# Kernel optimization log

Measured on AMD Instinct MI355X. Metric: run time of the kernel, lower is better.

Reference implementation:

```python
import jax, jax.numpy as jnp
import numpy as np

NUM_HEADS = 4
NUM_EXPERTS = 8
TOP_K = 2
AUX_W = 0.1


def setup_inputs() -> dict:
    key = jax.random.key(0)
    ks = jax.random.split(key, 16)
    B, W, C, T = 32, 64, 27, 2000
    E_EEG, H, S = 200, 256, 768
    D2 = 2 * H  # MoE input/hidden dim = 512
    s = 0.02

    def p(k, shape):
        return (jax.random.normal(k, shape, jnp.float32) * s)

    z = lambda *shape: jnp.zeros(shape, jnp.float32)
    return {
        "eeg_windows": jax.random.normal(ks[0], (B, W, C, T), jnp.float32),
        "padding_mask": jnp.zeros((B, W), bool),
        "smiles_emb": jax.random.normal(ks[1], (B, S), jnp.float32),
        # window encoder (linear stand-in): flatten (C*T) -> E_EEG
        "enc_W": p(ks[2], (C * T, E_EEG)), "enc_b": z(E_EEG),
        # aggregator (masked-mean + linear stand-in): E_EEG -> H
        "agg_W": p(ks[3], (E_EEG, H)), "agg_b": z(H),
        # smiles projection
        "smiles_W": p(ks[4], (S, H)), "smiles_b": z(H),
        # cross attention
        "Wq": p(ks[5], (H, H)), "bq": z(H),
        "Wk": p(ks[6], (H, H)), "bk": z(H),
        "Wv": p(ks[7], (H, H)), "bv": z(H),
        "Wo": p(ks[8], (H, H)), "bo": z(H),
        # MoE gate + experts
        "gate_W": p(ks[9], (D2, NUM_EXPERTS)), "gate_b": z(NUM_EXPERTS),
        "exp_W1": p(ks[10], (NUM_EXPERTS, D2, D2)), "exp_b1": z(NUM_EXPERTS, D2),
        "exp_W2": p(ks[11], (NUM_EXPERTS, D2, H)), "exp_b2": z(NUM_EXPERTS, H),
        # classifier
        "ln_g": jnp.ones((H,), jnp.float32), "ln_b": z(H),
        "cls_W": p(ks[12], (H, 2)), "cls_b": z(2),
    }


def reference(eeg_windows, padding_mask, smiles_emb, enc_W, enc_b, agg_W, agg_b,
              smiles_W, smiles_b, Wq, bq, Wk, bk, Wv, bv, Wo, bo,
              gate_W, gate_b, exp_W1, exp_b1, exp_W2, exp_b2,
              ln_g, ln_b, cls_W, cls_b):
    B, W, C, T = eeg_windows.shape
    H = agg_W.shape[1]
    dh = H // NUM_HEADS

    # --- window encoding (stand-in linear encoder) ---
    wemb = eeg_windows.reshape(B, W, C * T) @ enc_W + enc_b  # (B, W, E_EEG)

    # --- aggregator: masked mean pool over windows, then project ---
    valid = (~padding_mask).astype(wemb.dtype)[..., None]      # (B, W, 1)
    pooled = (wemb * valid).sum(1) / jnp.maximum(valid.sum(1), 1.0)
    eeg_emb = pooled @ agg_W + agg_b                           # (B, H)

    smiles_proj = smiles_emb @ smiles_W + smiles_b             # (B, H)

    # --- cross attention (single query token over single kv token) ---
    q = (eeg_emb @ Wq + bq).reshape(B, NUM_HEADS, dh)
    k = (smiles_proj @ Wk + bk).reshape(B, NUM_HEADS, dh)
    v = (smiles_proj @ Wv + bv).reshape(B, NUM_HEADS, dh)
    scores = (q * k).sum(-1, keepdims=True) / jnp.sqrt(jnp.float32(dh))
    attn = jnp.exp(scores - scores)  # softmax over a single key == 1
    attended = (attn * v).reshape(B, H) @ Wo + bo              # (B, H)

    fused = jnp.concatenate([attended, smiles_proj], axis=-1)  # (B, 2H)

    # --- sparse MoE: dense experts, top-k gate, gather, combine ---
    gate_probs = jax.nn.softmax(fused @ gate_W + gate_b, axis=-1)  # (B, E)
    topk_p, topk_i = jax.lax.top_k(gate_probs, TOP_K)
    topk_p = topk_p / topk_p.sum(-1, keepdims=True)
    h1 = jax.nn.gelu(jnp.einsum('bd,edh->beh', fused, exp_W1) + exp_b1,
                     approximate=False)
    expert_out = jnp.einsum('beh,eho->beo', h1, exp_W2) + exp_b2   # (B, E, H)
    sel = jnp.take_along_axis(expert_out, topk_i[:, :, None], axis=1)
    moe_out = (sel * topk_p[..., None]).sum(1)                     # (B, H)

    usage = gate_probs.mean(0)
    uniform = jnp.ones_like(usage) / usage.shape[-1]
    aux = (usage * jnp.log(uniform) - jnp.log(usage) * uniform).sum()

    # --- classifier: LayerNorm + Linear ---
    mu = moe_out.mean(-1, keepdims=True)
    var = moe_out.var(-1, keepdims=True)
    xn = (moe_out - mu) / jnp.sqrt(var + 1e-5)
    logits = (xn * ln_g + ln_b) @ cls_W + cls_b                    # (B, 2)
    return logits, aux * AUX_W
```

## Files before the change

kernel.cpp:

```cpp
#include <hip/hip_runtime.h>
#include <math.h>

#define HD 256
#define SD 768
#define D2 512
#define NE 8
#define NB 32
#define NBLK 256
#define NTHR 256
#define SFP 516

typedef float f32x4 __attribute__((ext_vector_type(4)));
typedef unsigned u32x4 __attribute__((ext_vector_type(4)));

__device__ __forceinline__ float gelu_exact(float x) {
    return 0.5f * x * (1.0f + erff(x * 0.70710678118654752f));
}

__device__ __forceinline__ void cstf(float* p, float v) {
    __hip_atomic_store(p, v, __ATOMIC_RELAXED, __HIP_MEMORY_SCOPE_AGENT);
}
__device__ __forceinline__ float cldf(const float* p) {
    return __hip_atomic_load(p, __ATOMIC_RELAXED, __HIP_MEMORY_SCOPE_AGENT);
}
__device__ __forceinline__ void csti(int* p, int v) {
    __hip_atomic_store(p, v, __ATOMIC_RELAXED, __HIP_MEMORY_SCOPE_AGENT);
}
__device__ __forceinline__ int cldi(const int* p) {
    return __hip_atomic_load(p, __ATOMIC_RELAXED, __HIP_MEMORY_SCOPE_AGENT);
}

__device__ __forceinline__ void stage16k(const float* __restrict__ gsrc,
                                         float* __restrict__ lds, int t)
{
    const f32x4* src = (const f32x4*)gsrc;
    f32x4 r[16];
    #pragma unroll
    for (int j = 0; j < 16; ++j) {
        const f32x4* p = src + (t + j * 256);
        asm volatile("global_load_dwordx4 %0, %1, off sc0 sc1"
                     : "=v"(r[j]) : "v"(p));
    }
    asm volatile("s_waitcnt vmcnt(0)" ::: "memory");
    __builtin_amdgcn_sched_barrier(0);
    #pragma unroll
    for (int j = 0; j < 16; ++j) {
        int q = t + j * 256;
        *(f32x4*)&lds[(q >> 7) * SFP + (q & 127) * 4] = r[j];
    }
}

__device__ __forceinline__ void post_slot(unsigned* slots, unsigned tok) {
    __syncthreads();
    if (threadIdx.x == 0)
        __hip_atomic_store(slots + blockIdx.x, tok, __ATOMIC_RELAXED,
                           __HIP_MEMORY_SCOPE_AGENT);
}

__device__ __forceinline__ void finish_full(const unsigned* slots,
                                            unsigned* gen, unsigned tok) {
    const int t = threadIdx.x;
    if (blockIdx.x == 0) {
        if (t < 64) {
            const u32x4* p = (const u32x4*)slots + t;
            for (;;) {
                u32x4 v;
                asm volatile("global_load_dwordx4 %0, %1, off sc0 sc1\n\t"
                             "s_waitcnt vmcnt(0)"
                             : "=&v"(v) : "v"(p) : "memory");
                bool ok = (v[0] == tok) & (v[1] == tok) &
                          (v[2] == tok) & (v[3] == tok);
                if (__ballot(ok) == ~0ull) break;
                __builtin_amdgcn_s_sleep(1);
            }
            if (t == 0)
                __hip_atomic_store(gen, tok, __ATOMIC_RELAXED,
                                   __HIP_MEMORY_SCOPE_AGENT);
        }
    } else {
        if (t == 0) {
            while (__hip_atomic_load(gen, __ATOMIC_RELAXED,
                                     __HIP_MEMORY_SCOPE_AGENT) != tok)
                __builtin_amdgcn_s_sleep(1);
        }
    }
    __builtin_amdgcn_fence(__ATOMIC_ACQUIRE, "workgroup");
    __syncthreads();
}

__device__ __forceinline__ void wait_subset(const unsigned* slots, int nq,
                                            unsigned tok) {
    if ((int)threadIdx.x < nq) {
        const u32x4* p = (const u32x4*)slots + threadIdx.x;
        for (;;) {
            u32x4 v;
            asm volatile("global_load_dwordx4 %0, %1, off sc0 sc1\n\t"
                         "s_waitcnt vmcnt(0)"
                         : "=&v"(v) : "v"(p) : "memory");
            if ((v[0] == tok) & (v[1] == tok) & (v[2] == tok) & (v[3] == tok))
                break;
            __builtin_amdgcn_s_sleep(2);
        }
    }
    __builtin_amdgcn_fence(__ATOMIC_ACQUIRE, "workgroup");
    __syncthreads();
}

#define S_F     0
#define S_W     16512
#define S_R2    (16512 + 8192)
#define S_RED   (16512 + 8192 + 4096)
#define S_SMALL (16512 + 8192 + 4096 + 256)
#define SMEM_F  (16512 + 8192 + 4096 + 256 + 16)

__global__ __launch_bounds__(256) void fused_all(
    const float* __restrict__ smiles,
    const float* __restrict__ sW, const float* __restrict__ sb,
    const float* __restrict__ Wv, const float* __restrict__ bv,
    const float* __restrict__ Wo, const float* __restrict__ bo,
    const float* __restrict__ gW, const float* __restrict__ gb,
    const float* __restrict__ W1, const float* __restrict__ b1,
    const float* __restrict__ W2, const float* __restrict__ b2,
    const float* __restrict__ lng, const float* __restrict__ lnb,
    const float* __restrict__ clsW, const float* __restrict__ clsb,
    float* __restrict__ proj, float* __restrict__ fused,
    float* __restrict__ probs, float* __restrict__ pn,
    int* __restrict__ sel, float* __restrict__ h1,
    float* __restrict__ eo,
    unsigned* __restrict__ slot0, unsigned* __restrict__ slot1,
    unsigned* __restrict__ slot2, unsigned* __restrict__ slot3,
    unsigned* __restrict__ gen, unsigned* __restrict__ LC,
    float* __restrict__ out)
{
    __shared__ __align__(16) float smem[SMEM_F];
    __shared__ unsigned s_lc;
    const int bid = blockIdx.x, t = threadIdx.x;

    if (t == 0)
        s_lc = __hip_atomic_load(LC, __ATOMIC_RELAXED, __HIP_MEMORY_SCOPE_AGENT);
    __syncthreads();
    const unsigned tb = s_lc * 2654435761u;

    {
        int r = bid >> 3, sl = bid & 7;
        float* s_in = smem + S_F;
        float* s_red = smem + S_RED;
        const float* srow = smiles + (size_t)r * SD;
        for (int i = t; i < SD / 4; i += NTHR)
            ((float4*)s_in)[i] = ((const float4*)srow)[i];
        __syncthreads();
        int c = t & 31, kq = t >> 5;
        float acc = 0.f;
        const float* wp = sW + (size_t)(kq * 96) * HD + sl * 32 + c;
        #pragma unroll 8
        for (int k = 0; k < 96; ++k)
            acc = fmaf(s_in[kq * 96 + k], wp[(size_t)k * HD], acc);
        s_red[t] = acc;
        __syncthreads();
        if (t < 32) {
            float s = 0.f;
            #pragma unroll
            for (int q = 0; q < 8; ++q) s += s_red[q * 32 + t];
            int col = sl * 32 + t;
            s += sb[col];
            cstf(proj + r * HD + col, s);
            cstf(fused + (size_t)r * 2 * HD + HD + col, s);
        }
    }
    post_slot(slot0, tb + 1u);

    if (bid < NB) {
        wait_subset(slot0 + bid * 8, 2, tb + 1u);
        int b = bid;
        float* s_p   = smem + S_F;
        float* s_v   = smem + S_F + 256;
        float* s_f2  = smem + S_F + 512;
        float* s_acc = smem + S_R2;
        float* s_red = smem + S_RED;
        float* s_gate = smem + S_SMALL;
        s_p[t] = cldf(proj + b * HD + t);
        __syncthreads();
        int ks = t >> 6, cg = t & 63;

        f32x4 av = {0.f, 0.f, 0.f, 0.f};
        #pragma unroll 16
        for (int kk = 0; kk < 64; ++kk) {
            int k = ks * 64 + kk;
            f32x4 w = *(const f32x4*)(Wv + (size_t)k * HD + cg * 4);
            av += s_p[k] * w;
        }
        *(f32x4*)&s_acc[ks * 256 + cg * 4] = av;
        __syncthreads();
        s_v[t] = s_acc[t] + s_acc[256 + t] + s_acc[512 + t] + s_acc[768 + t]
               + bv[t];
        __syncthreads();

        f32x4 ao = {0.f, 0.f, 0.f, 0.f};
        #pragma unroll 16
        for (int kk = 0; kk < 64; ++kk) {
            int k = ks * 64 + kk;
            f32x4 w = *(const f32x4*)(Wo + (size_t)k * HD + cg * 4);
            ao += s_v[k] * w;
        }
        *(f32x4*)&s_acc[ks * 256 + cg * 4] = ao;
        __syncthreads();
        float att = s_acc[t] + s_acc[256 + t] + s_acc[512 + t] + s_acc[768 + t]
                  + bo[t];
        s_f2[t] = att;
        s_f2[HD + t] = s_p[t];
        cstf(fused + (size_t)b * 2 * HD + t, att);
        __syncthreads();

        int e = t & 7, ch = t >> 3;
        float gp = 0.f;
        #pragma unroll
        for (int j = 0; j < 16; ++j) {
            int d = ch * 16 + j;
            gp = fmaf(s_f2[d], gW[d * NE + e], gp);
        }
        s_red[t] = gp;
        __syncthreads();
        for (int off = 128; off >= 8; off >>= 1) {
            if (t < off) s_red[t] += s_red[t + off];
            __syncthreads();
        }
        if (t < NE) s_gate[t] = s_red[t] + gb[t];
        __syncthreads();
        if (t == 0) {
            float m = s_gate[0];
            for (int i = 1; i < NE; ++i) m = fmaxf(m, s_gate[i]);
            float ex[NE], ssum = 0.f;
            for (int i = 0; i < NE; ++i) { ex[i] = expf(s_gate[i] - m); ssum += ex[i]; }
            float pr[NE];
            for (int i = 0; i < NE; ++i) { pr[i] = ex[i] / ssum; cstf(probs + b * NE + i, pr[i]); }
            int i1 = 0;
            for (int i = 1; i < NE; ++i) if (pr[i] > pr[i1]) i1 = i;
            int i2 = (i1 == 0) ? 1 : 0;
            for (int i = 0; i < NE; ++i) if (i != i1 && pr[i] > pr[i2]) i2 = i;
            float p1 = pr[i1], p2 = pr[i2], s12 = p1 + p2;
            csti(sel + b * 2 + 0, i1);
            csti(sel + b * 2 + 1, i2);
            cstf(pn + b * 2 + 0, p1 / s12);
            cstf(pn + b * 2 + 1, p2 / s12);
        }
    }
    post_slot(slot1, tb + 2u);

    {
        int e = bid >> 5, ct = bid & 31;
        float* s_w = smem + S_W;
        const float* Wb = W1 + (size_t)e * D2 * D2 + ct * 16;
        #pragma unroll
        for (int j = 0; j < 8; ++j) {
            int q = t + j * 256;
            int k = q >> 2, c4 = (q & 3) * 4;
            *(float4*)&s_w[k * 16 + c4] = *(const float4*)(Wb + (size_t)k * D2 + c4);
        }
    }
    finish_full(slot1, gen + 0, tb + 2u);

    {
        int e = bid >> 5, ct = bid & 31;
        float* s_f  = smem + S_F;
        float* s_w  = smem + S_W;
        float* s_r2 = smem + S_R2;
        stage16k(fused, s_f, t);
        __syncthreads();
        int ks = t >> 5, l = t & 31;
        int rg = l >> 2, c4g = l & 3;
        const float* wb = s_w + c4g * 4;
        int k0 = ks * 64;
        f32x4 a0 = {0.f,0.f,0.f,0.f}, a1 = a0, a2 = a0, a3 = a0;
        #pragma unroll 2
        for (int kq = 0; kq < 16; ++kq) {
            int k = k0 + kq * 4;
            f32x4 w0 = *(const f32x4*)&wb[(k + 0) * 16];
            f32x4 w1 = *(const f32x4*)&wb[(k + 1) * 16];
            f32x4 w2 = *(const f32x4*)&wb[(k + 2) * 16];
            f32x4 w3 = *(const f32x4*)&wb[(k + 3) * 16];
            f32x4 f0 = *(const f32x4*)&s_f[(rg     ) * SFP + k];
            f32x4 f1 = *(const f32x4*)&s_f[(rg +  8) * SFP + k];
            f32x4 f2 = *(const f32x4*)&s_f[(rg + 16) * SFP + k];
            f32x4 f3 = *(const f32x4*)&s_f[(rg + 24) * SFP + k];
            a0 += f0[0]*w0 + f0[1]*w1 + f0[2]*w2 + f0[3]*w3;
            a1 += f1[0]*w0 + f1[1]*w1 + f1[2]*w2 + f1[3]*w3;
            a2 += f2[0]*w0 + f2[1]*w1 + f2[2]*w2 + f2[3]*w3;
            a3 += f3[0]*w0 + f3[1]*w1 + f3[2]*w2 + f3[3]*w3;
        }
        *(f32x4*)&s_r2[ks * 512 + (rg     ) * 16 + c4g * 4] = a0;
        *(f32x4*)&s_r2[ks * 512 + (rg +  8) * 16 + c4g * 4] = a1;
        *(f32x4*)&s_r2[ks * 512 + (rg + 16) * 16 + c4g * 4] = a2;
        *(f32x4*)&s_r2[ks * 512 + (rg + 24) * 16 + c4g * 4] = a3;
        __syncthreads();
        #pragma unroll
        for (int o = 0; o < 2; ++o) {
            int outi = t * 2 + o;
            float s = 0.f;
            #pragma unroll
            for (int p = 0; p < 8; ++p) s += s_r2[p * 512 + outi];
            int r = outi >> 4, cl = outi & 15;
            int col = ct * 16 + cl;
            cstf(h1 + ((size_t)e * NB + r) * D2 + col,
                 gelu_exact(s + b1[e * D2 + col]));
        }
    }
    post_slot(slot2, tb + 3u);

    if (bid >= 128) {
        post_slot(slot3, tb + 4u);
        return;
    }

    {
        int e = bid >> 4, ct = bid & 15;
        float* s_w = smem + S_W;
        const float* Wb = W2 + (size_t)e * D2 * HD + ct * 16;
        #pragma unroll
        for (int j = 0; j < 8; ++j) {
            int q = t + j * 256;
            int k = q >> 2, c4 = (q & 3) * 4;
            *(float4*)&s_w[k * 16 + c4] = *(const float4*)(Wb + (size_t)k * HD + c4);
        }
    }
    finish_full(slot2, gen + 1, tb + 3u);

    {
        int e = bid >> 4, ct = bid & 15;
        float* s_f  = smem + S_F;
        float* s_w  = smem + S_W;
        float* s_r2 = smem + S_R2;
        stage16k(h1 + (size_t)e * NB * D2, s_f, t);
        __syncthreads();
        int ks = t >> 5, l = t & 31;
        int rg = l >> 2, c4g = l & 3;
        const float* wb = s_w + c4g * 4;
        int k0 = ks * 64;
        f32x4 a0 = {0.f,0.f,0.f,0.f}, a1 = a0, a2 = a0, a3 = a0;
        #pragma unroll 2
        for (int kq = 0; kq < 16; ++kq) {
            int k = k0 + kq * 4;
            f32x4 w0 = *(const f32x4*)&wb[(k + 0) * 16];
            f32x4 w1 = *(const f32x4*)&wb[(k + 1) * 16];
            f32x4 w2 = *(const f32x4*)&wb[(k + 2) * 16];
            f32x4 w3 = *(const f32x4*)&wb[(k + 3) * 16];
            f32x4 f0 = *(const f32x4*)&s_f[(rg     ) * SFP + k];
            f32x4 f1 = *(const f32x4*)&s_f[(rg +  8) * SFP + k];
            f32x4 f2 = *(const f32x4*)&s_f[(rg + 16) * SFP + k];
            f32x4 f3 = *(const f32x4*)&s_f[(rg + 24) * SFP + k];
            a0 += f0[0]*w0 + f0[1]*w1 + f0[2]*w2 + f0[3]*w3;
            a1 += f1[0]*w0 + f1[1]*w1 + f1[2]*w2 + f1[3]*w3;
            a2 += f2[0]*w0 + f2[1]*w1 + f2[2]*w2 + f2[3]*w3;
            a3 += f3[0]*w0 + f3[1]*w1 + f3[2]*w2 + f3[3]*w3;
        }
        *(f32x4*)&s_r2[ks * 512 + (rg     ) * 16 + c4g * 4] = a0;
        *(f32x4*)&s_r2[ks * 512 + (rg +  8) * 16 + c4g * 4] = a1;
        *(f32x4*)&s_r2[ks * 512 + (rg + 16) * 16 + c4g * 4] = a2;
        *(f32x4*)&s_r2[ks * 512 + (rg + 24) * 16 + c4g * 4] = a3;
        __syncthreads();
        #pragma unroll
        for (int o = 0; o < 2; ++o) {
            int outi = t * 2 + o;
            float s = 0.f;
            #pragma unroll
            for (int p = 0; p < 8; ++p) s += s_r2[p * 512 + outi];
            int r = outi >> 4, cl = outi & 15;
            int col = ct * 16 + cl;
            cstf(eo + ((size_t)e * NB + r) * HD + col, s + b2[e * HD + col]);
        }
    }
    post_slot(slot3, tb + 4u);
    if (bid >= NB) return;

    finish_full(slot3, gen + 2, tb + 4u);

    {
        int b = bid;
        float* s_red = smem + S_RED;
        float* s_stats = smem + S_SMALL;
        int e0 = cldi(sel + b * 2 + 0), e1 = cldi(sel + b * 2 + 1);
        float p0 = cldf(pn + b * 2 + 0), p1 = cldf(pn + b * 2 + 1);
        float moe = p0 * cldf(eo + ((size_t)e0 * NB + b) * HD + t)
                  + p1 * cldf(eo + ((size_t)e1 * NB + b) * HD + t);

        s_red[t] = moe; __syncthreads();
        for (int off = 128; off > 0; off >>= 1) {
            if (t < off) s_red[t] += s_red[t + off];
            __syncthreads();
        }
        if (t == 0) s_stats[0] = s_red[0] * (1.f / HD);
        __syncthreads();
        float mu = s_stats[0];
        float d = moe - mu;

        s_red[t] = d * d; __syncthreads();
        for (int off = 128; off > 0; off >>= 1) {
            if (t < off) s_red[t] += s_red[t + off];
            __syncthreads();
        }
        if (t == 0) s_stats[1] = s_red[0] * (1.f / HD);
        __syncthreads();

        float xn = d * rsqrtf(s_stats[1] + 1e-5f);
        float y = fmaf(xn, lng[t], lnb[t]);

        s_red[t] = y * clsW[t * 2 + 0]; __syncthreads();
        for (int off = 128; off > 0; off >>= 1) {
            if (t < off) s_red[t] += s_red[t + off];
            __syncthreads();
        }
        if (t == 0) s_stats[2] = s_red[0] + clsb[0];
        __syncthreads();

        s_red[t] = y * clsW[t * 2 + 1]; __syncthreads();
        for (int off = 128; off > 0; off >>= 1) {
            if (t < off) s_red[t] += s_red[t + off];
            __syncthreads();
        }
        if (t == 0) {
            out[b * 2 + 0] = s_stats[2];
            out[b * 2 + 1] = s_red[0] + clsb[1];
        }

        if (bid == 0) {
            __syncthreads();
            s_red[t] = cldf(probs + t);
            __syncthreads();
            for (int off = 128; off >= 8; off >>= 1) {
                if (t < off) s_red[t] += s_red[t + off];
                __syncthreads();
            }
            if (t == 0) {
                float aux = 0.f;
                for (int e = 0; e < NE; ++e) {
                    float u = s_red[e] * (1.f / 32.f);
                    aux += u * logf(0.125f) - logf(u) * 0.125f;
                }
                out[64] = 0.1f * aux;
            }
        }
    }

    if (bid == 0 && t == 0)
        __hip_atomic_store(LC, s_lc + 1u, __ATOMIC_RELAXED,
                           __HIP_MEMORY_SCOPE_AGENT);
}

extern "C" void kernel_launch(void* const* d_in, const int* in_sizes, int n_in,
                              void* d_out, int out_size, void* d_ws, size_t ws_size,
                              hipStream_t stream) {
    (void)in_sizes; (void)n_in; (void)out_size; (void)ws_size;
    const float* smiles = (const float*)d_in[2];
    const float* sW  = (const float*)d_in[7];
    const float* sb  = (const float*)d_in[8];
    const float* Wv  = (const float*)d_in[13];
    const float* bv  = (const float*)d_in[14];
    const float* Wo  = (const float*)d_in[15];
    const float* bo  = (const float*)d_in[16];
    const float* gW  = (const float*)d_in[17];
    const float* gb  = (const float*)d_in[18];
    const float* W1  = (const float*)d_in[19];
    const float* b1  = (const float*)d_in[20];
    const float* W2  = (const float*)d_in[21];
    const float* b2  = (const float*)d_in[22];
    const float* lng = (const float*)d_in[23];
    const float* lnb = (const float*)d_in[24];
    const float* cW  = (const float*)d_in[25];
    const float* cb  = (const float*)d_in[26];
    float* out = (float*)d_out;
    float* ws  = (float*)d_ws;

    float*    proj  = ws;
    float*    fused = ws + 8192;
    float*    probs = ws + 24576;
    float*    pn    = ws + 24832;
    int*      sel   = (int*)(ws + 24896);
    float*    h1    = ws + 24960;
    float*    eo    = ws + 156032;
    unsigned* slot0 = (unsigned*)(ws + 221568);
    unsigned* slot1 = (unsigned*)(ws + 221824);
    unsigned* slot2 = (unsigned*)(ws + 222080);
    unsigned* slot3 = (unsigned*)(ws + 222336);
    unsigned* gen   = (unsigned*)(ws + 222592);
    unsigned* LC    = (unsigned*)(ws + 222596);

    fused_all<<<NBLK, NTHR, 0, stream>>>(
        smiles, sW, sb, Wv, bv, Wo, bo, gW, gb, W1, b1, W2, b2,
        lng, lnb, cW, cb,
        proj, fused, probs, pn, sel, h1, eo,
        slot0, slot1, slot2, slot3, gen, LC, out);
}
```

Before: 38.82 us.

## Replace full grid barriers with per-expert dependency waits in MoE stages

Swaps the grid-wide barriers before the second expert GEMM and the combine stage for targeted waits. Each expert-W2 block now waits only on the slot2 flags of the 16 blocks that produced its expert's h1. Each batch row waits only on the slot3 flags for its two selected experts. Block 0 also waits on all slot2 slots before bumping the launch counter, so slot reuse across launches stays safe. This removes stalls on unrelated blocks, but correctness now depends on the slot indexing matching the producer layout.

```diff
diff --git a/kernel.cpp b/kernel.cpp
--- a/kernel.cpp
+++ b/kernel.cpp
@@ -92,6 +92,25 @@
                                             unsigned tok) {
     if ((int)threadIdx.x < nq) {
         const u32x4* p = (const u32x4*)slots + threadIdx.x;
+        for (;;) {
+            u32x4 v;
+            asm volatile("global_load_dwordx4 %0, %1, off sc0 sc1\n\t"
+                         "s_waitcnt vmcnt(0)"
+                         : "=&v"(v) : "v"(p) : "memory");
+            if ((v[0] == tok) & (v[1] == tok) & (v[2] == tok) & (v[3] == tok))
+                break;
+            __builtin_amdgcn_s_sleep(2);
+        }
+    }
+    __builtin_amdgcn_fence(__ATOMIC_ACQUIRE, "workgroup");
+    __syncthreads();
+}
+
+__device__ __forceinline__ void wait_two_experts(const unsigned* slots,
+                                                 int ea, int eb, unsigned tok) {
+    if (threadIdx.x < 8) {
+        int es = (threadIdx.x < 4) ? ea : eb;
+        const u32x4* p = (const u32x4*)slots + es * 4 + (threadIdx.x & 3);
         for (;;) {
             u32x4 v;
             asm volatile("global_load_dwordx4 %0, %1, off sc0 sc1\n\t"
@@ -305,11 +324,7 @@
         }
     }
     post_slot(slot2, tb + 3u);
-
-    if (bid >= 128) {
-        post_slot(slot3, tb + 4u);
-        return;
-    }
+    if (bid >= 128) return;
 
     {
         int e = bid >> 4, ct = bid & 15;
@@ -322,7 +337,10 @@
             *(float4*)&s_w[k * 16 + c4] = *(const float4*)(Wb + (size_t)k * HD + c4);
         }
     }
-    finish_full(slot2, gen + 1, tb + 3u);
+    {
+        int e = bid >> 4;
+        wait_subset(slot2 + e * 32, 8, tb + 3u);
+    }
 
     {
         int e = bid >> 4, ct = bid & 15;
@@ -371,14 +389,15 @@
     post_slot(slot3, tb + 4u);
     if (bid >= NB) return;
 
-    finish_full(slot3, gen + 2, tb + 4u);
-
     {
         int b = bid;
         float* s_red = smem + S_RED;
         float* s_stats = smem + S_SMALL;
         int e0 = cldi(sel + b * 2 + 0), e1 = cldi(sel + b * 2 + 1);
         float p0 = cldf(pn + b * 2 + 0), p1 = cldf(pn + b * 2 + 1);
+
+        wait_two_experts(slot3, e0, e1, tb + 4u);
+
         float moe = p0 * cldf(eo + ((size_t)e0 * NB + b) * HD + t)
                   + p1 * cldf(eo + ((size_t)e1 * NB + b) * HD + t);
 
@@ -440,9 +459,12 @@
         }
     }
 
-    if (bid == 0 && t == 0)
-        __hip_atomic_store(LC, s_lc + 1u, __ATOMIC_RELAXED,
-                           __HIP_MEMORY_SCOPE_AGENT);
+    if (bid == 0) {
+        wait_subset(slot2, 64, tb + 3u);
+        if (t == 0)
+            __hip_atomic_store(LC, s_lc + 1u, __ATOMIC_RELAXED,
+                               __HIP_MEMORY_SCOPE_AGENT);
+    }
 }
 
 extern "C" void kernel_launch(void* const* d_in, const int* in_sizes, int n_in,
```

Result: faster. 37.87 us (-2.4%).
